# Optimization experiments

Hardware: AMD Instinct MI355X
Metric: run time of the kernel (lower is better)

The kernel has to match this reference:

```python
import jax, jax.numpy as jnp
import numpy as np

M = 10000      # spans with antecedents
KMAX = 30      # max antecedents per span
N = 12000      # total candidate spans (rows of g_i)
GDIM = 512     # span embedding dim
DDIM, GEDIM, SDIM = 20, 20, 20  # distance / genre / speaker embed dims
HID = 150      # Score hidden dim
GIJ = 3 * GDIM + DDIM + GEDIM + SDIM  # 1596
NDIST, NGENRE, NSPK = 10, 7, 3


def setup_inputs() -> dict:
    rng = np.random.default_rng(0)
    lengths = rng.integers(1, KMAX + 1, size=M)           # antecedents per span
    P = int(lengths.sum())
    seg_ids = np.repeat(np.arange(1, M + 1), lengths).astype(np.int32)  # segment 0 is the leading empty split
    pos_in_seg = np.concatenate([np.arange(l) for l in lengths]).astype(np.int32)
    seg_lengths = np.concatenate([[0], lengths]).astype(np.int32)        # [S], S = M+1
    mention_ids = rng.integers(0, N, size=P).astype(np.int32)
    antecedent_ids = rng.integers(0, N, size=P).astype(np.int32)
    dist_idx = rng.integers(0, NDIST, size=P).astype(np.int32)
    genre_idx = rng.integers(0, NGENRE, size=P).astype(np.int32)
    speaker_idx = rng.integers(0, NSPK, size=P).astype(np.int32)

    ks = jax.random.split(jax.random.key(0), 12)
    sc = lambda d: 1.0 / np.sqrt(d)
    return {
        'g_i': jax.random.normal(ks[0], (N, GDIM), jnp.float32),
        'mention_scores': jax.random.normal(ks[1], (N, 1), jnp.float32),
        'dist_emb': jax.random.normal(ks[2], (NDIST, DDIM), jnp.float32),
        'genre_emb': jax.random.normal(ks[3], (NGENRE, GEDIM), jnp.float32),
        'speaker_emb': jax.random.normal(ks[4], (NSPK, SDIM), jnp.float32),
        'W1': jax.random.normal(ks[5], (GIJ, HID), jnp.float32) * sc(GIJ),
        'b1': jnp.zeros((HID,), jnp.float32),
        'W2': jax.random.normal(ks[6], (HID, HID), jnp.float32) * sc(HID),
        'b2': jnp.zeros((HID,), jnp.float32),
        'W3': jax.random.normal(ks[7], (HID, 1), jnp.float32) * sc(HID),
        'b3': jnp.zeros((1,), jnp.float32),
        'mention_ids': jnp.asarray(mention_ids),
        'antecedent_ids': jnp.asarray(antecedent_ids),
        'dist_idx': jnp.asarray(dist_idx),
        'genre_idx': jnp.asarray(genre_idx),
        'speaker_idx': jnp.asarray(speaker_idx),
        'seg_ids': jnp.asarray(seg_ids),
        'pos_in_seg': jnp.asarray(pos_in_seg),
        'seg_lengths': jnp.asarray(seg_lengths),
    }


def reference(g_i, mention_scores, dist_emb, genre_emb, speaker_emb,
              W1, b1, W2, b2, W3, b3,
              mention_ids, antecedent_ids, dist_idx, genre_idx, speaker_idx,
              seg_ids, pos_in_seg, seg_lengths):
    # phi = cat(distance, genre, speaker) side features, [P, 60]
    phi = jnp.concatenate([dist_emb[dist_idx], genre_emb[genre_idx], speaker_emb[speaker_idx]], axis=1)
    i_g = g_i[mention_ids]      # [P, GDIM] irregular gather
    j_g = g_i[antecedent_ids]   # [P, GDIM]
    pairs = jnp.concatenate([i_g, j_g, i_g * j_g, phi], axis=1)  # [P, GIJ]
    # 3-layer MLP scorer (dropout is identity at inference)
    h = jax.nn.relu(pairs @ W1 + b1)
    h = jax.nn.relu(h @ W2 + b2)
    s_ij = (h @ W3 + b3)[:, 0]  # [P]
    coref = mention_scores[mention_ids, 0] + mention_scores[antecedent_ids, 0] + s_ij  # [P]
    # variable-length segment softmax with epsilon=0 appended, padded with 1000
    S = seg_lengths.shape[0]
    dense = jnp.full((S, KMAX + 1), -jnp.inf, jnp.float32)
    dense = dense.at[seg_ids, pos_in_seg].set(coref)
    dense = dense.at[jnp.arange(S), seg_lengths].set(0.0)  # epsilon slot
    probs = jax.nn.softmax(dense, axis=1)  # -inf slots -> 0
    col = jnp.arange(KMAX + 1)
    probs = jnp.where(col[None, :] > seg_lengths[:, None], 1000.0, probs)  # pad value 1000
    return probs  # [S, KMAX+1]
```

## Files before the change

### kernel.cpp

```cpp
#include <hip/hip_runtime.h>
#include <stdint.h>

#define GDIM   512
#define HID    150
#define HIDP   160
#define NROWS  12000
#define KP1    31
#define BMP    128
#define BMF    128

typedef __attribute__((ext_vector_type(4))) float f32x4;
typedef __attribute__((ext_vector_type(2))) float f32x2;
typedef long i64;

__device__ __forceinline__ unsigned short f2bf(float x){
    unsigned int u = __float_as_uint(x);
    return (unsigned short)((u + 0x7fffu + ((u >> 16) & 1u)) >> 16);
}
__device__ __forceinline__ float bf2f(unsigned short u){
    return __uint_as_float(((unsigned int)u) << 16);
}
__device__ __forceinline__ i64 u2l(uint2 v){ return __builtin_bit_cast(i64, v); }
__device__ __forceinline__ f32x4 mfma8(i64 a, i64 b, f32x4 c){
    return __builtin_amdgcn_mfma_f32_16x16x32_fp8_fp8(a, b, c, 0, 0, 0);
}
__device__ __forceinline__ uint2 f8mulpk(uint2 m, uint2 a){
    f32x2 m0 = __builtin_amdgcn_cvt_pk_f32_fp8(m.x, false);
    f32x2 m1 = __builtin_amdgcn_cvt_pk_f32_fp8(m.x, true);
    f32x2 m2 = __builtin_amdgcn_cvt_pk_f32_fp8(m.y, false);
    f32x2 m3 = __builtin_amdgcn_cvt_pk_f32_fp8(m.y, true);
    f32x2 a0 = __builtin_amdgcn_cvt_pk_f32_fp8(a.x, false);
    f32x2 a1 = __builtin_amdgcn_cvt_pk_f32_fp8(a.x, true);
    f32x2 a2 = __builtin_amdgcn_cvt_pk_f32_fp8(a.y, false);
    f32x2 a3 = __builtin_amdgcn_cvt_pk_f32_fp8(a.y, true);
    unsigned int r0 = 0, r1 = 0;
    r0 = __builtin_amdgcn_cvt_pk_fp8_f32(m0[0]*a0[0], m0[1]*a0[1], r0, false);
    r0 = __builtin_amdgcn_cvt_pk_fp8_f32(m1[0]*a1[0], m1[1]*a1[1], r0, true);
    r1 = __builtin_amdgcn_cvt_pk_fp8_f32(m2[0]*a2[0], m2[1]*a2[1], r1, false);
    r1 = __builtin_amdgcn_cvt_pk_fp8_f32(m3[0]*a3[0], m3[1]*a3[1], r1, true);
    return (uint2){r0, r1};
}
__device__ __forceinline__ void glds16(const void* g, void* l){
    __builtin_amdgcn_global_load_lds(
        (const __attribute__((address_space(1))) unsigned int*)g,
        (__attribute__((address_space(3))) unsigned int*)l, 16, 0, 0);
}

__global__ void k_prep0(const float* __restrict__ g, unsigned char* __restrict__ g8,
                        int* __restrict__ hist, int4* __restrict__ recs,
                        const float* __restrict__ W1, unsigned char* __restrict__ W18,
                        const float* __restrict__ W2, unsigned char* __restrict__ W28,
                        const float* __restrict__ de, const float* __restrict__ ge,
                        const float* __restrict__ se, const float* __restrict__ b1,
                        const float* __restrict__ W3, const float* __restrict__ b2,
                        unsigned short* __restrict__ PhiW,
                        float* __restrict__ w3p, float* __restrict__ b2p, int P){
    int i = blockIdx.x * blockDim.x + threadIdx.x;
    if (i < NROWS) hist[i] = 0;
    if (i < BMF) recs[P + i] = (int4){0, 0, (int)0x80000000, 0};
    if (i < 30720){
        int s = i / 10240, r = i % 10240;
        int n = r >> 6, gi = r & 63;
        int gdst = gi ^ (n & 7);
        int k0 = s * 512 + gi * 8;
        float x[8];
        #pragma unroll
        for (int e = 0; e < 8; e++) x[e] = (n < HID) ? W1[(size_t)(k0 + e) * HID + n] : 0.f;
        unsigned int d0 = 0, d1 = 0;
        d0 = __builtin_amdgcn_cvt_pk_fp8_f32(x[0], x[1], d0, false);
        d0 = __builtin_amdgcn_cvt_pk_fp8_f32(x[2], x[3], d0, true);
        d1 = __builtin_amdgcn_cvt_pk_fp8_f32(x[4], x[5], d1, false);
        d1 = __builtin_amdgcn_cvt_pk_fp8_f32(x[6], x[7], d1, true);
        *reinterpret_cast<uint2*>(W18 + (size_t)s * 81920 + n * 512 + gdst * 8) = (uint2){d0, d1};
    }
    if (i < 6912){
        int n2 = i / 42, kd = (i % 42) * 4;
        float y[4];
        #pragma unroll
        for (int e = 0; e < 4; e++){
            int k = kd + e;
            y[e] = (n2 < HID && k < HID) ? W2[(size_t)k * HID + n2] : 0.f;
        }
        unsigned int d = 0;
        d = __builtin_amdgcn_cvt_pk_fp8_f32(y[0], y[1], d, false);
        d = __builtin_amdgcn_cvt_pk_fp8_f32(y[2], y[3], d, true);
        reinterpret_cast<unsigned int*>(W28)[i] = d;
    }
    if (i < NROWS * 32){
        int lh = i & 3, kt = (i >> 2) & 7, row = i >> 5;
        const float* src = g + (size_t)row * 512 + kt * 64 + lh * 8;
        float4 x0 = *reinterpret_cast<const float4*>(src);
        float4 x1 = *reinterpret_cast<const float4*>(src + 4);
        float4 x2 = *reinterpret_cast<const float4*>(src + 32);
        float4 x3 = *reinterpret_cast<const float4*>(src + 36);
        uint4 o; unsigned int d;
        d = 0; d = __builtin_amdgcn_cvt_pk_fp8_f32(x0.x, x0.y, d, false);
        d = __builtin_amdgcn_cvt_pk_fp8_f32(x0.z, x0.w, d, true);  o.x = d;
        d = 0; d = __builtin_amdgcn_cvt_pk_fp8_f32(x1.x, x1.y, d, false);
        d = __builtin_amdgcn_cvt_pk_fp8_f32(x1.z, x1.w, d, true);  o.y = d;
        d = 0; d = __builtin_amdgcn_cvt_pk_fp8_f32(x2.x, x2.y, d, false);
        d = __builtin_amdgcn_cvt_pk_fp8_f32(x2.z, x2.w, d, true);  o.z = d;
        d = 0; d = __builtin_amdgcn_cvt_pk_fp8_f32(x3.x, x3.y, d, false);
        d = __builtin_amdgcn_cvt_pk_fp8_f32(x3.z, x3.w, d, true);  o.w = d;
        *reinterpret_cast<uint4*>(g8 + (size_t)row * 512 + kt * 64 + lh * 16) = o;
    } else if (i < NROWS * 32 + 33600){
        int j = i - NROWS * 32;
        int c = j / HIDP, h = j - c * HIDP;
        int si = c % 3, gi2 = (c / 3) % 7, di = c / 21;
        float acc = 0.f;
        if (h < HID){
            acc = b1[h];
            #pragma unroll
            for (int dd = 0; dd < 20; dd++) acc += de[di*20 + dd] * W1[(size_t)(1536 + dd) * HID + h];
            #pragma unroll
            for (int dd = 0; dd < 20; dd++) acc += ge[gi2*20 + dd] * W1[(size_t)(1556 + dd) * HID + h];
            #pragma unroll
            for (int dd = 0; dd < 20; dd++) acc += se[si*20 + dd] * W1[(size_t)(1576 + dd) * HID + h];
        }
        PhiW[c * HIDP + h] = f2bf(acc);
    } else if (i < NROWS * 32 + 33600 + HIDP){
        int h = i - NROWS * 32 - 33600;
        w3p[h] = (h < HID) ? W3[h] : 0.f;
        b2p[h] = (h < HID) ? b2[h] : 0.f;
    }
}

__global__ void k_hist(const int* __restrict__ mid, int* __restrict__ hist, int P){
    int p = blockIdx.x * blockDim.x + threadIdx.x;
    if (p < P) atomicAdd(&hist[mid[p]], 1);
}
__global__ void k_scan(const int* __restrict__ hist, int* __restrict__ offsw, int nb){
    __shared__ int part[1024];
    int t = threadIdx.x;
    int chunk = (nb + 1023) / 1024;
    int lo = t * chunk, hi = lo + chunk; if (hi > nb) hi = nb;
    int s = 0;
    for (int b = lo; b < hi; b++) s += hist[b];
    part[t] = s;
    __syncthreads();
    for (int d = 1; d < 1024; d <<= 1){
        int v = (t >= d) ? part[t - d] : 0;
        __syncthreads();
        part[t] += v;
        __syncthreads();
    }
    int run = part[t] - s;
    for (int b = lo; b < hi; b++){ offsw[b] = run; run += hist[b]; }
}
__global__ void k_scatter(const int* __restrict__ mident, const int* __restrict__ antid,
                          const int* __restrict__ di, const int* __restrict__ gi, const int* __restrict__ si,
                          const int* __restrict__ seg, const int* __restrict__ pos, const float* __restrict__ ms,
                          int* __restrict__ offsw, int4* __restrict__ recs, int P){
    int p = blockIdx.x * blockDim.x + threadIdx.x;
    if (p >= P) return;
    int m = mident[p], a = antid[p];
    int idx = atomicAdd(&offsw[m], 1);
    int combo = (di[p] * 7 + gi[p]) * 3 + si[p];
    int meta = (combo << 19) | (seg[p] << 5) | pos[p];
    int4 r; r.x = m; r.y = a; r.z = meta; r.w = __float_as_int(ms[m] + ms[a]);
    recs[idx] = r;
}

__global__ __launch_bounds__(256) void k_proj(const unsigned char* __restrict__ g8,
                                              const unsigned char* __restrict__ W18,
                                              unsigned char* __restrict__ out){
    __shared__ __align__(16) char smem[81920];
    const unsigned char* Wt = W18 + (size_t)blockIdx.y * 81920;
    unsigned char* outh = out + (size_t)blockIdx.y * NROWS * HIDP;
    int tid = threadIdx.x, lane = tid & 63, w = tid >> 6;
    int l15 = lane & 15, lh = lane >> 4;
    int swz8 = (l15 & 7) << 3;
    int row0 = blockIdx.x * BMP;

    int r0 = row0 + 32*w + l15;       int r0c = (r0 < NROWS) ? r0 : NROWS - 1;
    int r1 = r0 + 16;                 int r1c = (r1 < NROWS) ? r1 : NROWS - 1;
    const unsigned char* gp0 = g8 + (size_t)r0c * GDIM + lh * 16;
    const unsigned char* gp1 = g8 + (size_t)r1c * GDIM + lh * 16;

    #pragma unroll
    for (int i = 0; i < 20; i++){
        int c = w * 20 + i;
        glds16(Wt + c * 1024 + lane * 16, smem + c * 1024);
    }

    f32x4 acc1[10][2];
    #pragma unroll
    for (int t = 0; t < 10; t++){ acc1[t][0] = (f32x4){0,0,0,0}; acc1[t][1] = (f32x4){0,0,0,0}; }

    asm volatile("s_waitcnt vmcnt(0)" ::: "memory");
    __builtin_amdgcn_s_barrier();

    uint4 R0 = *reinterpret_cast<const uint4*>(gp0);
    uint4 R1 = *reinterpret_cast<const uint4*>(gp1);
    #pragma unroll
    for (int kt = 0; kt < 8; kt++){
        uint4 N0, N1;
        if (kt < 7){
            N0 = *reinterpret_cast<const uint4*>(gp0 + (kt+1)*64);
            N1 = *reinterpret_cast<const uint4*>(gp1 + (kt+1)*64);
        }
        i64 a00 = u2l((uint2){R0.x, R0.y}), a01 = u2l((uint2){R0.z, R0.w});
        i64 a10 = u2l((uint2){R1.x, R1.y}), a11 = u2l((uint2){R1.z, R1.w});
        __builtin_amdgcn_s_setprio(1);
        #pragma unroll
        for (int t = 0; t < 10; t++){
            int rowb = (t*16 + l15) * 512;
            i64 b0 = *reinterpret_cast<const i64*>(&smem[rowb + ((kt*64 +  0 + lh*8) ^ swz8)]);
            i64 b1 = *reinterpret_cast<const i64*>(&smem[rowb + ((kt*64 + 32 + lh*8) ^ swz8)]);
            acc1[t][0] = mfma8(b0, a00, acc1[t][0]);
            acc1[t][1] = mfma8(b0, a10, acc1[t][1]);
            acc1[t][0] = mfma8(b1, a01, acc1[t][0]);
            acc1[t][1] = mfma8(b1, a11, acc1[t][1]);
        }
        __builtin_amdgcn_s_setprio(0);
        R0 = N0; R1 = N1;
    }

    #pragma unroll
    for (int rf = 0; rf < 2; rf++){
        int row = row0 + 32*w + 16*rf + l15;
        if (row < NROWS){
            #pragma unroll
            for (int t = 0; t < 10; t++){
                f32x4 a = acc1[t][rf];
                unsigned int dw = 0;
                dw = __builtin_amdgcn_cvt_pk_fp8_f32(a[0], a[1], dw, false);
                dw = __builtin_amdgcn_cvt_pk_fp8_f32(a[2], a[3], dw, true);
                *reinterpret_cast<unsigned int*>(outh + (size_t)row * HIDP + 16*t + 4*lh) = dw;
            }
        }
    }
}

__global__ __launch_bounds__(256) void k_fused(
    const unsigned char* __restrict__ g8,
    const unsigned char* __restrict__ W1c8, const unsigned char* __restrict__ W28,
    const unsigned short* __restrict__ PhiW, const unsigned char* __restrict__ Am,
    const unsigned char* __restrict__ Aa,
    const float* __restrict__ w3p, const float* __restrict__ b2p, const float* __restrict__ b3,
    const int4* __restrict__ recs,
    float* __restrict__ dense)
{
    __shared__ __align__(16) char smem[81920];
    int tid = threadIdx.x, lane = tid & 63, w = tid >> 6;
    int l15 = lane & 15, lh = lane >> 4;
    int swz8 = (l15 & 7) << 3;

    int nwg = gridDim.x, orig = blockIdx.x, bid = orig;
    if (nwg >= 8){
        int q = nwg >> 3, r = nwg & 7;
        int xcd = orig & 7, lid = orig >> 3;
        bid = (xcd < r ? xcd * (q + 1) : r * (q + 1) + (xcd - r) * q) + lid;
    }
    int p0 = bid * BMF;

    int4 rec0 = recs[p0 + 32*w + l15];
    int4 rec1 = recs[p0 + 32*w + 16 + l15];

    const unsigned char* gm0 = g8 + (size_t)rec0.x * GDIM + lh * 16;
    const unsigned char* ga0 = g8 + (size_t)rec0.y * GDIM + lh * 16;
    const unsigned char* gm1 = g8 + (size_t)rec1.x * GDIM + lh * 16;
    const unsigned char* ga1 = g8 + (size_t)rec1.y * GDIM + lh * 16;

    #pragma unroll
    for (int i = 0; i < 20; i++){
        int c = w * 20 + i;
        glds16(W1c8 + c * 1024 + lane * 16, smem + c * 1024);
    }

    f32x4 acc1[10][2];
    #pragma unroll
    for (int t = 0; t < 10; t++){ acc1[t][0] = (f32x4){0,0,0,0}; acc1[t][1] = (f32x4){0,0,0,0}; }

    asm volatile("s_waitcnt vmcnt(0)" ::: "memory");
    __builtin_amdgcn_s_barrier();

    uint4 Rm0 = *reinterpret_cast<const uint4*>(gm0);
    uint4 Ra0 = *reinterpret_cast<const uint4*>(ga0);
    uint4 Rm1 = *reinterpret_cast<const uint4*>(gm1);
    uint4 Ra1 = *reinterpret_cast<const uint4*>(ga1);
    #pragma unroll
    for (int kt = 0; kt < 8; kt++){
        uint4 Nm0, Na0, Nm1, Na1;
        if (kt < 7){
            Nm0 = *reinterpret_cast<const uint4*>(gm0 + (kt+1)*64);
            Na0 = *reinterpret_cast<const uint4*>(ga0 + (kt+1)*64);
            Nm1 = *reinterpret_cast<const uint4*>(gm1 + (kt+1)*64);
            Na1 = *reinterpret_cast<const uint4*>(ga1 + (kt+1)*64);
        }
        uint2 p00 = f8mulpk((uint2){Rm0.x, Rm0.y}, (uint2){Ra0.x, Ra0.y});
        uint2 p01 = f8mulpk((uint2){Rm0.z, Rm0.w}, (uint2){Ra0.z, Ra0.w});
        uint2 p10 = f8mulpk((uint2){Rm1.x, Rm1.y}, (uint2){Ra1.x, Ra1.y});
        uint2 p11 = f8mulpk((uint2){Rm1.z, Rm1.w}, (uint2){Ra1.z, Ra1.w});
        i64 lp00 = u2l(p00), lp01 = u2l(p01), lp10 = u2l(p10), lp11 = u2l(p11);
        __builtin_amdgcn_s_setprio(1);
        #pragma unroll
        for (int t = 0; t < 10; t++){
            int rowb = (t*16 + l15) * 512;
            i64 b0 = *reinterpret_cast<const i64*>(&smem[rowb + ((kt*64 +  0 + lh*8) ^ swz8)]);
            i64 b1 = *reinterpret_cast<const i64*>(&smem[rowb + ((kt*64 + 32 + lh*8) ^ swz8)]);
            acc1[t][0] = mfma8(b0, lp00, acc1[t][0]);
            acc1[t][1] = mfma8(b0, lp10, acc1[t][1]);
            acc1[t][0] = mfma8(b1, lp01, acc1[t][0]);
            acc1[t][1] = mfma8(b1, lp11, acc1[t][1]);
        }
        __builtin_amdgcn_s_setprio(0);
        Rm0 = Nm0; Ra0 = Na0; Rm1 = Nm1; Ra1 = Na1;
    }

    asm volatile("s_waitcnt lgkmcnt(0)" ::: "memory");
    __builtin_amdgcn_s_barrier();

    #pragma unroll
    for (int i = 0; i < 7; i++){
        int c = w * 7 + i;
        if (c < 27) glds16(W28 + c * 1024 + lane * 16, smem + 21504 + c * 1024);
    }

    #pragma unroll
    for (int rf = 0; rf < 2; rf++){
        int4 rc = rf ? rec1 : rec0;
        int pr = 32*w + 16*rf + l15;
        const unsigned char* amp = Am + (size_t)rc.x * HIDP;
        const unsigned char* aap = Aa + (size_t)rc.y * HIDP;
        int combo = (rc.z >> 19) & 0xFF;
        const unsigned short* php = PhiW + (size_t)combo * HIDP;
        char* h1row = smem + pr * 168;
        #pragma unroll
        for (int t = 0; t < 10; t++){
            int h0 = 16*t + 4*lh;
            unsigned int amd = *reinterpret_cast<const unsigned int*>(amp + h0);
            unsigned int aad = *reinterpret_cast<const unsigned int*>(aap + h0);
            ushort4 ph4 = *reinterpret_cast<const ushort4*>(php + h0);
            f32x2 amL = __builtin_amdgcn_cvt_pk_f32_fp8(amd, false);
            f32x2 amH = __builtin_amdgcn_cvt_pk_f32_fp8(amd, true);
            f32x2 aaL = __builtin_amdgcn_cvt_pk_f32_fp8(aad, false);
            f32x2 aaH = __builtin_amdgcn_cvt_pk_f32_fp8(aad, true);
            f32x4 a = acc1[t][rf];
            float v0 = fmaxf(a[0] + amL[0] + aaL[0] + bf2f(ph4.x), 0.f);
            float v1 = fmaxf(a[1] + amL[1] + aaL[1] + bf2f(ph4.y), 0.f);
            float v2 = fmaxf(a[2] + amH[0] + aaH[0] + bf2f(ph4.z), 0.f);
            float v3 = fmaxf(a[3] + amH[1] + aaH[1] + bf2f(ph4.w), 0.f);
            unsigned int dw = 0;
            dw = __builtin_amdgcn_cvt_pk_fp8_f32(v0, v1, dw, false);
            dw = __builtin_amdgcn_cvt_pk_fp8_f32(v2, v3, dw, true);
            *reinterpret_cast<unsigned int*>(h1row + h0) = dw;
        }
    }

    asm volatile("s_waitcnt vmcnt(0) lgkmcnt(0)" ::: "memory");
    __builtin_amdgcn_s_barrier();

    f32x4 acc2[10][2];
    #pragma unroll
    for (int t = 0; t < 10; t++){ acc2[t][0] = (f32x4){0,0,0,0}; acc2[t][1] = (f32x4){0,0,0,0}; }
    const char* w2b = smem + 21504;
    __builtin_amdgcn_s_setprio(1);
    #pragma unroll
    for (int k2 = 0; k2 < 5; k2++){
        i64 h0f = *reinterpret_cast<const i64*>(smem + (32*w + l15)      * 168 + k2*32 + lh*8);
        i64 h1f = *reinterpret_cast<const i64*>(smem + (32*w + 16 + l15) * 168 + k2*32 + lh*8);
        #pragma unroll
        for (int t = 0; t < 10; t++){
            i64 wf = *reinterpret_cast<const i64*>(w2b + (16*t + l15) * 168 + k2*32 + lh*8);
            acc2[t][0] = mfma8(wf, h0f, acc2[t][0]);
            acc2[t][1] = mfma8(wf, h1f, acc2[t][1]);
        }
    }
    __builtin_amdgcn_s_setprio(0);

    float b3v = b3[0];
    #pragma unroll
    for (int rf = 0; rf < 2; rf++){
        int4 rc = rf ? rec1 : rec0;
        float s = 0.f;
        #pragma unroll
        for (int t = 0; t < 10; t++){
            f32x4 w3v = *reinterpret_cast<const f32x4*>(w3p + 16*t + 4*lh);
            f32x4 b2v = *reinterpret_cast<const f32x4*>(b2p + 16*t + 4*lh);
            f32x4 a = acc2[t][rf];
            s += fmaxf(a[0] + b2v[0], 0.f) * w3v[0];
            s += fmaxf(a[1] + b2v[1], 0.f) * w3v[1];
            s += fmaxf(a[2] + b2v[2], 0.f) * w3v[2];
            s += fmaxf(a[3] + b2v[3], 0.f) * w3v[3];
        }
        s += __shfl_xor(s, 16);
        s += __shfl_xor(s, 32);
        if (!(rc.z & 0x80000000) && lh == 0){
            float val = s + b3v + __int_as_float(rc.w);
            dense[(size_t)((rc.z >> 5) & 0x3FFF) * KP1 + (rc.z & 31)] = val;
        }
    }
}

__global__ void k_softmax(const float* __restrict__ dense, const int* __restrict__ seg_lengths,
                          float* __restrict__ out, int S){
    int wid = threadIdx.x >> 6, lane = threadIdx.x & 63;
    int s = blockIdx.x * 4 + wid;
    if (s >= S) return;
    int len = seg_lengths[s];
    float ninf = -__builtin_inff();
    float val = ninf;
    if (lane < KP1) val = (lane < len) ? dense[(size_t)s * KP1 + lane] : ((lane == len) ? 0.f : ninf);
    float m = val;
    #pragma unroll
    for (int msk = 1; msk < 64; msk <<= 1) m = fmaxf(m, __shfl_xor(m, msk));
    float e = expf(val - m);
    float sum = e;
    #pragma unroll
    for (int msk = 1; msk < 64; msk <<= 1) sum += __shfl_xor(sum, msk);
    if (lane < KP1) out[(size_t)s * KP1 + lane] = (lane > len) ? 1000.f : (e / sum);
}

extern "C" void kernel_launch(void* const* d_in, const int* in_sizes, int n_in,
                              void* d_out, int out_size, void* d_ws, size_t ws_size,
                              hipStream_t stream){
    const float* g_i        = (const float*)d_in[0];
    const float* ms         = (const float*)d_in[1];
    const float* dist_emb   = (const float*)d_in[2];
    const float* genre_emb  = (const float*)d_in[3];
    const float* spk_emb    = (const float*)d_in[4];
    const float* W1         = (const float*)d_in[5];
    const float* b1         = (const float*)d_in[6];
    const float* W2         = (const float*)d_in[7];
    const float* b2         = (const float*)d_in[8];
    const float* W3         = (const float*)d_in[9];
    const float* b3         = (const float*)d_in[10];
    const int* mention_ids  = (const int*)d_in[11];
    const int* antecedent_ids = (const int*)d_in[12];
    const int* dist_idx     = (const int*)d_in[13];
    const int* genre_idx    = (const int*)d_in[14];
    const int* spk_idx      = (const int*)d_in[15];
    const int* seg_ids      = (const int*)d_in[16];
    const int* pos_in_seg   = (const int*)d_in[17];
    const int* seg_lengths  = (const int*)d_in[18];
    int P = in_sizes[11];
    int S = in_sizes[18];

    char* ws = (char*)d_ws;
    unsigned char* W18   = (unsigned char*)(ws + 0);
    unsigned char* W28   = (unsigned char*)(ws + 245760);
    unsigned short* PhiW = (unsigned short*)(ws + 273408);
    float* w3pad         = (float*)(ws + 340608);
    float* b2pad         = (float*)(ws + 341248);
    unsigned char* g8    = (unsigned char*)(ws + 341888);
    unsigned char* Am8   = (unsigned char*)(ws + 6485888);
    unsigned char* Aa8   = (unsigned char*)(ws + 8405888);
    int* hist            = (int*)(ws + 10325888);
    int* offsw           = (int*)(ws + 10373888);
    int4* recs           = (int4*)(ws + 10421888);
    float* dense         = (float*)(ws + 13000192);

    int prep_threads = NROWS * 32 + 33600 + HIDP;
    k_prep0<<<(prep_threads + 255)/256, 256, 0, stream>>>(g_i, g8, hist, recs, W1, W18, W2, W28,
        dist_emb, genre_emb, spk_emb, b1, W3, b2, PhiW, w3pad, b2pad, P);
    k_hist<<<(P + 255)/256, 256, 0, stream>>>(mention_ids, hist, P);
    k_scan<<<1, 1024, 0, stream>>>(hist, offsw, NROWS);
    k_scatter<<<(P + 255)/256, 256, 0, stream>>>(mention_ids, antecedent_ids, dist_idx, genre_idx,
        spk_idx, seg_ids, pos_in_seg, ms, offsw, recs, P);

    k_proj<<<dim3((NROWS + BMP - 1)/BMP, 2), 256, 0, stream>>>(g8, W18, Am8);

    k_fused<<<(P + BMF - 1)/BMF, 256, 0, stream>>>(g8, W18 + 2*81920, W28, PhiW,
        Am8, Aa8, w3pad, b2pad, b3, recs, dense);

    k_softmax<<<(S + 3)/4, 256, 0, stream>>>(dense, seg_lengths, (float*)d_out, S);
}
```

Measured before the change: 111.4 us.

## Drop per-row projection kernel; compute full W1 GEMM per pair in fused kernel

Removes the k_proj kernel that precomputed g_i·W1 for the mention and antecedent slices per unique row. The fused kernel now runs all three W1 slices (mention, antecedent, product) per pair, loading each 80KB weight slice into LDS in three phases. The tile shrinks to 64 pairs per block with launch_bounds(…,2) to raise occupancy. This trades a separate launch and its gathered fp8 intermediate reads for roughly three times the layer-1 MFMA work per pair plus extra barriers and LDS reloads.

```diff
diff --git a/kernel.cpp b/kernel.cpp
--- a/kernel.cpp
+++ b/kernel.cpp
@@ -6,8 +6,7 @@
 #define HIDP   160
 #define NROWS  12000
 #define KP1    31
-#define BMP    128
-#define BMF    128
+#define BMF    64
 
 typedef __attribute__((ext_vector_type(4))) float f32x4;
 typedef __attribute__((ext_vector_type(2))) float f32x2;
@@ -57,7 +56,7 @@
                         float* __restrict__ w3p, float* __restrict__ b2p, int P){
     int i = blockIdx.x * blockDim.x + threadIdx.x;
     if (i < NROWS) hist[i] = 0;
-    if (i < BMF) recs[P + i] = (int4){0, 0, (int)0x80000000, 0};
+    if (i < 128) recs[P + i] = (int4){0, 0, (int)0x80000000, 0};
     if (i < 30720){
         int s = i / 10240, r = i % 10240;
         int n = r >> 6, gi = r & 63;
@@ -161,82 +160,10 @@
     recs[idx] = r;
 }
 
-__global__ __launch_bounds__(256) void k_proj(const unsigned char* __restrict__ g8,
-                                              const unsigned char* __restrict__ W18,
-                                              unsigned char* __restrict__ out){
-    __shared__ __align__(16) char smem[81920];
-    const unsigned char* Wt = W18 + (size_t)blockIdx.y * 81920;
-    unsigned char* outh = out + (size_t)blockIdx.y * NROWS * HIDP;
-    int tid = threadIdx.x, lane = tid & 63, w = tid >> 6;
-    int l15 = lane & 15, lh = lane >> 4;
-    int swz8 = (l15 & 7) << 3;
-    int row0 = blockIdx.x * BMP;
-
-    int r0 = row0 + 32*w + l15;       int r0c = (r0 < NROWS) ? r0 : NROWS - 1;
-    int r1 = r0 + 16;                 int r1c = (r1 < NROWS) ? r1 : NROWS - 1;
-    const unsigned char* gp0 = g8 + (size_t)r0c * GDIM + lh * 16;
-    const unsigned char* gp1 = g8 + (size_t)r1c * GDIM + lh * 16;
-
-    #pragma unroll
-    for (int i = 0; i < 20; i++){
-        int c = w * 20 + i;
-        glds16(Wt + c * 1024 + lane * 16, smem + c * 1024);
-    }
-
-    f32x4 acc1[10][2];
-    #pragma unroll
-    for (int t = 0; t < 10; t++){ acc1[t][0] = (f32x4){0,0,0,0}; acc1[t][1] = (f32x4){0,0,0,0}; }
-
-    asm volatile("s_waitcnt vmcnt(0)" ::: "memory");
-    __builtin_amdgcn_s_barrier();
-
-    uint4 R0 = *reinterpret_cast<const uint4*>(gp0);
-    uint4 R1 = *reinterpret_cast<const uint4*>(gp1);
-    #pragma unroll
-    for (int kt = 0; kt < 8; kt++){
-        uint4 N0, N1;
-        if (kt < 7){
-            N0 = *reinterpret_cast<const uint4*>(gp0 + (kt+1)*64);
-            N1 = *reinterpret_cast<const uint4*>(gp1 + (kt+1)*64);
-        }
-        i64 a00 = u2l((uint2){R0.x, R0.y}), a01 = u2l((uint2){R0.z, R0.w});
-        i64 a10 = u2l((uint2){R1.x, R1.y}), a11 = u2l((uint2){R1.z, R1.w});
-        __builtin_amdgcn_s_setprio(1);
-        #pragma unroll
-        for (int t = 0; t < 10; t++){
-            int rowb = (t*16 + l15) * 512;
-            i64 b0 = *reinterpret_cast<const i64*>(&smem[rowb + ((kt*64 +  0 + lh*8) ^ swz8)]);
-            i64 b1 = *reinterpret_cast<const i64*>(&smem[rowb + ((kt*64 + 32 + lh*8) ^ swz8)]);
-            acc1[t][0] = mfma8(b0, a00, acc1[t][0]);
-            acc1[t][1] = mfma8(b0, a10, acc1[t][1]);
-            acc1[t][0] = mfma8(b1, a01, acc1[t][0]);
-            acc1[t][1] = mfma8(b1, a11, acc1[t][1]);
-        }
-        __builtin_amdgcn_s_setprio(0);
-        R0 = N0; R1 = N1;
-    }
-
-    #pragma unroll
-    for (int rf = 0; rf < 2; rf++){
-        int row = row0 + 32*w + 16*rf + l15;
-        if (row < NROWS){
-            #pragma unroll
-            for (int t = 0; t < 10; t++){
-                f32x4 a = acc1[t][rf];
-                unsigned int dw = 0;
-                dw = __builtin_amdgcn_cvt_pk_fp8_f32(a[0], a[1], dw, false);
-                dw = __builtin_amdgcn_cvt_pk_fp8_f32(a[2], a[3], dw, true);
-                *reinterpret_cast<unsigned int*>(outh + (size_t)row * HIDP + 16*t + 4*lh) = dw;
-            }
-        }
-    }
-}
-
-__global__ __launch_bounds__(256) void k_fused(
+__global__ __launch_bounds__(256, 2) void k_fused(
     const unsigned char* __restrict__ g8,
-    const unsigned char* __restrict__ W1c8, const unsigned char* __restrict__ W28,
-    const unsigned short* __restrict__ PhiW, const unsigned char* __restrict__ Am,
-    const unsigned char* __restrict__ Aa,
+    const unsigned char* __restrict__ W18, const unsigned char* __restrict__ W28,
+    const unsigned short* __restrict__ PhiW,
     const float* __restrict__ w3p, const float* __restrict__ b2p, const float* __restrict__ b3,
     const int4* __restrict__ recs,
     float* __restrict__ dense)
@@ -254,93 +181,87 @@
     }
     int p0 = bid * BMF;
 
-    int4 rec0 = recs[p0 + 32*w + l15];
-    int4 rec1 = recs[p0 + 32*w + 16 + l15];
-
-    const unsigned char* gm0 = g8 + (size_t)rec0.x * GDIM + lh * 16;
-    const unsigned char* ga0 = g8 + (size_t)rec0.y * GDIM + lh * 16;
-    const unsigned char* gm1 = g8 + (size_t)rec1.x * GDIM + lh * 16;
-    const unsigned char* ga1 = g8 + (size_t)rec1.y * GDIM + lh * 16;
+    int4 rec = recs[p0 + 16*w + l15];
+    const unsigned char* gm = g8 + (size_t)rec.x * GDIM + lh * 16;
+    const unsigned char* ga = g8 + (size_t)rec.y * GDIM + lh * 16;
 
     #pragma unroll
     for (int i = 0; i < 20; i++){
         int c = w * 20 + i;
-        glds16(W1c8 + c * 1024 + lane * 16, smem + c * 1024);
-    }
-
-    f32x4 acc1[10][2];
-    #pragma unroll
-    for (int t = 0; t < 10; t++){ acc1[t][0] = (f32x4){0,0,0,0}; acc1[t][1] = (f32x4){0,0,0,0}; }
-
-    asm volatile("s_waitcnt vmcnt(0)" ::: "memory");
-    __builtin_amdgcn_s_barrier();
-
-    uint4 Rm0 = *reinterpret_cast<const uint4*>(gm0);
-    uint4 Ra0 = *reinterpret_cast<const uint4*>(ga0);
-    uint4 Rm1 = *reinterpret_cast<const uint4*>(gm1);
-    uint4 Ra1 = *reinterpret_cast<const uint4*>(ga1);
+        glds16(W18 + c * 1024 + lane * 16, smem + c * 1024);
+    }
+
+    uint4 Rm[8], Ra[8];
     #pragma unroll
     for (int kt = 0; kt < 8; kt++){
-        uint4 Nm0, Na0, Nm1, Na1;
-        if (kt < 7){
-            Nm0 = *reinterpret_cast<const uint4*>(gm0 + (kt+1)*64);
-            Na0 = *reinterpret_cast<const uint4*>(ga0 + (kt+1)*64);
-            Nm1 = *reinterpret_cast<const uint4*>(gm1 + (kt+1)*64);
-            Na1 = *reinterpret_cast<const uint4*>(ga1 + (kt+1)*64);
-        }
-        uint2 p00 = f8mulpk((uint2){Rm0.x, Rm0.y}, (uint2){Ra0.x, Ra0.y});
-        uint2 p01 = f8mulpk((uint2){Rm0.z, Rm0.w}, (uint2){Ra0.z, Ra0.w});
-        uint2 p10 = f8mulpk((uint2){Rm1.x, Rm1.y}, (uint2){Ra1.x, Ra1.y});
-        uint2 p11 = f8mulpk((uint2){Rm1.z, Rm1.w}, (uint2){Ra1.z, Ra1.w});
-        i64 lp00 = u2l(p00), lp01 = u2l(p01), lp10 = u2l(p10), lp11 = u2l(p11);
+        Rm[kt] = *reinterpret_cast<const uint4*>(gm + kt*64);
+        Ra[kt] = *reinterpret_cast<const uint4*>(ga + kt*64);
+    }
+
+    f32x4 acc1[10];
+    #pragma unroll
+    for (int t = 0; t < 10; t++) acc1[t] = (f32x4){0,0,0,0};
+
+    #pragma unroll
+    for (int ph = 0; ph < 3; ph++){
+        asm volatile("s_waitcnt vmcnt(0)" ::: "memory");
+        __builtin_amdgcn_s_barrier();
         __builtin_amdgcn_s_setprio(1);
         #pragma unroll
-        for (int t = 0; t < 10; t++){
-            int rowb = (t*16 + l15) * 512;
-            i64 b0 = *reinterpret_cast<const i64*>(&smem[rowb + ((kt*64 +  0 + lh*8) ^ swz8)]);
-            i64 b1 = *reinterpret_cast<const i64*>(&smem[rowb + ((kt*64 + 32 + lh*8) ^ swz8)]);
-            acc1[t][0] = mfma8(b0, lp00, acc1[t][0]);
-            acc1[t][1] = mfma8(b0, lp10, acc1[t][1]);
-            acc1[t][0] = mfma8(b1, lp01, acc1[t][0]);
-            acc1[t][1] = mfma8(b1, lp11, acc1[t][1]);
+        for (int kt = 0; kt < 8; kt++){
+            i64 x0, x1;
+            if (ph == 0){
+                x0 = u2l((uint2){Rm[kt].x, Rm[kt].y});
+                x1 = u2l((uint2){Rm[kt].z, Rm[kt].w});
+            } else if (ph == 1){
+                x0 = u2l((uint2){Ra[kt].x, Ra[kt].y});
+                x1 = u2l((uint2){Ra[kt].z, Ra[kt].w});
+            } else {
+                uint2 pp0 = f8mulpk((uint2){Rm[kt].x, Rm[kt].y}, (uint2){Ra[kt].x, Ra[kt].y});
+                uint2 pp1 = f8mulpk((uint2){Rm[kt].z, Rm[kt].w}, (uint2){Ra[kt].z, Ra[kt].w});
+                x0 = u2l(pp0); x1 = u2l(pp1);
+            }
+            #pragma unroll
+            for (int t = 0; t < 10; t++){
+                int rowb = (t*16 + l15) * 512;
+                i64 b0 = *reinterpret_cast<const i64*>(&smem[rowb + ((kt*64 +  0 + lh*8) ^ swz8)]);
+                i64 b1 = *reinterpret_cast<const i64*>(&smem[rowb + ((kt*64 + 32 + lh*8) ^ swz8)]);
+                acc1[t] = mfma8(b0, x0, acc1[t]);
+                acc1[t] = mfma8(b1, x1, acc1[t]);
+            }
         }
         __builtin_amdgcn_s_setprio(0);
-        Rm0 = Nm0; Ra0 = Na0; Rm1 = Nm1; Ra1 = Na1;
-    }
-
-    asm volatile("s_waitcnt lgkmcnt(0)" ::: "memory");
-    __builtin_amdgcn_s_barrier();
+        asm volatile("s_waitcnt lgkmcnt(0)" ::: "memory");
+        __builtin_amdgcn_s_barrier();
+        if (ph < 2){
+            #pragma unroll
+            for (int i = 0; i < 20; i++){
+                int c = w * 20 + i;
+                glds16(W18 + (size_t)(ph+1) * 81920 + c * 1024 + lane * 16, smem + c * 1024);
+            }
+        }
+    }
 
     #pragma unroll
     for (int i = 0; i < 7; i++){
         int c = w * 7 + i;
-        if (c < 27) glds16(W28 + c * 1024 + lane * 16, smem + 21504 + c * 1024);
-    }
-
-    #pragma unroll
-    for (int rf = 0; rf < 2; rf++){
-        int4 rc = rf ? rec1 : rec0;
-        int pr = 32*w + 16*rf + l15;
-        const unsigned char* amp = Am + (size_t)rc.x * HIDP;
-        const unsigned char* aap = Aa + (size_t)rc.y * HIDP;
-        int combo = (rc.z >> 19) & 0xFF;
+        if (c < 27) glds16(W28 + c * 1024 + lane * 16, smem + 10752 + c * 1024);
+    }
+
+    {
+        int pr = 16*w + l15;
+        int combo = (rec.z >> 19) & 0xFF;
         const unsigned short* php = PhiW + (size_t)combo * HIDP;
         char* h1row = smem + pr * 168;
         #pragma unroll
         for (int t = 0; t < 10; t++){
             int h0 = 16*t + 4*lh;
-            unsigned int amd = *reinterpret_cast<const unsigned int*>(amp + h0);
-            unsigned int aad = *reinterpret_cast<const unsigned int*>(aap + h0);
             ushort4 ph4 = *reinterpret_cast<const ushort4*>(php + h0);
-            f32x2 amL = __builtin_amdgcn_cvt_pk_f32_fp8(amd, false);
-            f32x2 amH = __builtin_amdgcn_cvt_pk_f32_fp8(amd, true);
-            f32x2 aaL = __builtin_amdgcn_cvt_pk_f32_fp8(aad, false);
-            f32x2 aaH = __builtin_amdgcn_cvt_pk_f32_fp8(aad, true);
-            f32x4 a = acc1[t][rf];
-            float v0 = fmaxf(a[0] + amL[0] + aaL[0] + bf2f(ph4.x), 0.f);
-            float v1 = fmaxf(a[1] + amL[1] + aaL[1] + bf2f(ph4.y), 0.f);
-            float v2 = fmaxf(a[2] + amH[0] + aaH[0] + bf2f(ph4.z), 0.f);
-            float v3 = fmaxf(a[3] + amH[1] + aaH[1] + bf2f(ph4.w), 0.f);
+            f32x4 a = acc1[t];
+            float v0 = fmaxf(a[0] + bf2f(ph4.x), 0.f);
+            float v1 = fmaxf(a[1] + bf2f(ph4.y), 0.f);
+            float v2 = fmaxf(a[2] + bf2f(ph4.z), 0.f);
+            float v3 = fmaxf(a[3] + bf2f(ph4.w), 0.f);
             unsigned int dw = 0;
             dw = __builtin_amdgcn_cvt_pk_fp8_f32(v0, v1, dw, false);
             dw = __builtin_amdgcn_cvt_pk_fp8_f32(v2, v3, dw, true);
@@ -351,45 +272,39 @@
     asm volatile("s_waitcnt vmcnt(0) lgkmcnt(0)" ::: "memory");
     __builtin_amdgcn_s_barrier();
 
-    f32x4 acc2[10][2];
-    #pragma unroll
-    for (int t = 0; t < 10; t++){ acc2[t][0] = (f32x4){0,0,0,0}; acc2[t][1] = (f32x4){0,0,0,0}; }
-    const char* w2b = smem + 21504;
+    f32x4 acc2[10];
+    #pragma unroll
+    for (int t = 0; t < 10; t++) acc2[t] = (f32x4){0,0,0,0};
+    const char* w2b = smem + 10752;
     __builtin_amdgcn_s_setprio(1);
     #pragma unroll
     for (int k2 = 0; k2 < 5; k2++){
-        i64 h0f = *reinterpret_cast<const i64*>(smem + (32*w + l15)      * 168 + k2*32 + lh*8);
-        i64 h1f = *reinterpret_cast<const i64*>(smem + (32*w + 16 + l15) * 168 + k2*32 + lh*8);
+        i64 hf = *reinterpret_cast<const i64*>(smem + (16*w + l15) * 168 + k2*32 + lh*8);
         #pragma unroll
         for (int t = 0; t < 10; t++){
             i64 wf = *reinterpret_cast<const i64*>(w2b + (16*t + l15) * 168 + k2*32 + lh*8);
-            acc2[t][0] = mfma8(wf, h0f, acc2[t][0]);
-            acc2[t][1] = mfma8(wf, h1f, acc2[t][1]);
+            acc2[t] = mfma8(wf, hf, acc2[t]);
         }
     }
     __builtin_amdgcn_s_setprio(0);
 
     float b3v = b3[0];
-    #pragma unroll
-    for (int rf = 0; rf < 2; rf++){
-        int4 rc = rf ? rec1 : rec0;
-        float s = 0.f;
-        #pragma unroll
-        for (int t = 0; t < 10; t++){
-            f32x4 w3v = *reinterpret_cast<const f32x4*>(w3p + 16*t + 4*lh);
-            f32x4 b2v = *reinterpret_cast<const f32x4*>(b2p + 16*t + 4*lh);
-            f32x4 a = acc2[t][rf];
-            s += fmaxf(a[0] + b2v[0], 0.f) * w3v[0];
-            s += fmaxf(a[1] + b2v[1], 0.f) * w3v[1];
-            s += fmaxf(a[2] + b2v[2], 0.f) * w3v[2];
-            s += fmaxf(a[3] + b2v[3], 0.f) * w3v[3];
-        }
-        s += __shfl_xor(s, 16);
-        s += __shfl_xor(s, 32);
-        if (!(rc.z & 0x80000000) && lh == 0){
-            float val = s + b3v + __int_as_float(rc.w);
-            dense[(size_t)((rc.z >> 5) & 0x3FFF) * KP1 + (rc.z & 31)] = val;
-        }
+    float s = 0.f;
+    #pragma unroll
+    for (int t = 0; t < 10; t++){
+        f32x4 w3v = *reinterpret_cast<const f32x4*>(w3p + 16*t + 4*lh);
+        f32x4 b2v = *reinterpret_cast<const f32x4*>(b2p + 16*t + 4*lh);
+        f32x4 a = acc2[t];
+        s += fmaxf(a[0] + b2v[0], 0.f) * w3v[0];
+        s += fmaxf(a[1] + b2v[1], 0.f) * w3v[1];
+        s += fmaxf(a[2] + b2v[2], 0.f) * w3v[2];
+        s += fmaxf(a[3] + b2v[3], 0.f) * w3v[3];
+    }
+    s += __shfl_xor(s, 16);
+    s += __shfl_xor(s, 32);
+    if (!(rec.z & 0x80000000) && lh == 0){
+        float val = s + b3v + __int_as_float(rec.w);
+        dense[(size_t)((rec.z >> 5) & 0x3FFF) * KP1 + (rec.z & 31)] = val;
     }
 }
 
@@ -444,12 +359,10 @@
     float* w3pad         = (float*)(ws + 340608);
     float* b2pad         = (float*)(ws + 341248);
     unsigned char* g8    = (unsigned char*)(ws + 341888);
-    unsigned char* Am8   = (unsigned char*)(ws + 6485888);
-    unsigned char* Aa8   = (unsigned char*)(ws + 8405888);
-    int* hist            = (int*)(ws + 10325888);
-    int* offsw           = (int*)(ws + 10373888);
-    int4* recs           = (int4*)(ws + 10421888);
-    float* dense         = (float*)(ws + 13000192);
+    int* hist            = (int*)(ws + 6485888);
+    int* offsw           = (int*)(ws + 6533888);
+    int4* recs           = (int4*)(ws + 6581888);
+    float* dense         = (float*)(ws + 9160192);
 
     int prep_threads = NROWS * 32 + 33600 + HIDP;
     k_prep0<<<(prep_threads + 255)/256, 256, 0, stream>>>(g_i, g8, hist, recs, W1, W18, W2, W28,
@@ -459,10 +372,8 @@
     k_scatter<<<(P + 255)/256, 256, 0, stream>>>(mention_ids, antecedent_ids, dist_idx, genre_idx,
         spk_idx, seg_ids, pos_in_seg, ms, offsw, recs, P);
 
-    k_proj<<<dim3((NROWS + BMP - 1)/BMP, 2), 256, 0, stream>>>(g8, W18, Am8);
-
-    k_fused<<<(P + BMF - 1)/BMF, 256, 0, stream>>>(g8, W18 + 2*81920, W28, PhiW,
-        Am8, Aa8, w3pad, b2pad, b3, recs, dense);
+    k_fused<<<(P + BMF - 1)/BMF, 256, 0, stream>>>(g8, W18, W28, PhiW,
+        w3pad, b2pad, b3, recs, dense);
 
     k_softmax<<<(S + 3)/4, 256, 0, stream>>>(dense, seg_lengths, (float*)d_out, S);
 }
```

Result: slower. 153.4 us (+37.7%).
